# Optimization experiments

Measured on AMD Instinct MI355X. Metric: run time of the kernel, lower is better.

Reference implementation:

```python
import jax, jax.numpy as jnp
import numpy as np

N, E, DIN, DH, DC = 50000, 1600000, 128, 128, 40
EPS = 1e-5  # BatchNorm eps


def _seg_sum(v, idx, n):
    return jax.ops.segment_sum(v, idx, num_segments=n)


def setup_inputs() -> dict:
    key = jax.random.key(0)
    ks = jax.random.split(key, 24)
    rn = lambda i, shp, s=0.05: jax.random.normal(ks[i], shp, jnp.float32) * s
    return {
        "x": jax.random.normal(ks[0], (N, DIN), jnp.float32),
        "src": jax.random.randint(ks[1], (E,), 0, N, jnp.int32),
        "dst": jax.random.randint(ks[2], (E,), 0, N, jnp.int32),
        # CoNet layer 1 (in -> hidden)
        "w11s": rn(3, (DIN, DH)), "w11n": rn(4, (DIN, DH)), "b11": jnp.zeros((DH,), jnp.float32),
        "w12": rn(5, (DIN, DH)), "b12": jnp.zeros((DH,), jnp.float32),
        "w13": rn(6, (DIN, DH)), "a13l": rn(7, (DH,)), "a13r": rn(8, (DH,)), "b13": jnp.zeros((DH,), jnp.float32),
        "cw1": jax.random.uniform(ks[9], (3,), jnp.float32, 0.5, 1.5),
        # BatchNorm1d
        "g": jnp.ones((DH,), jnp.float32), "be": jnp.zeros((DH,), jnp.float32),
        # CoNet layer 2 (hidden -> out)
        "w21s": rn(10, (DH, DC)), "w21n": rn(11, (DH, DC)), "b21": jnp.zeros((DC,), jnp.float32),
        "w22": rn(12, (DH, DC)), "b22": jnp.zeros((DC,), jnp.float32),
        "w23": rn(13, (DH, DC)), "a23l": rn(14, (DC,)), "a23r": rn(15, (DC,)), "b23": jnp.zeros((DC,), jnp.float32),
        "cw2": jax.random.uniform(ks[16], (3,), jnp.float32, 0.5, 1.5),
    }


def conet(x, src, dst, ws, wn, bs, wg, bg, wa, al, ar, ba, cw):
    """AFFN CoNet: SAGE(mean) + GCN + GAT(1 head), fused by normalized weights."""
    n = x.shape[0]
    ones = jnp.ones((src.shape[0],), x.dtype)
    indeg = _seg_sum(ones, dst, n)   # in-degree per node
    outdeg = _seg_sum(ones, src, n)  # out-degree per node

    # --- SAGEConv, mean aggregator: fc_self(x) + fc_neigh(mean_neigh(x)) ---
    nei = _seg_sum(x[src], dst, n) / jnp.maximum(indeg, 1.0)[:, None]
    x1 = x @ ws + nei @ wn + bs

    ns = jnp.maximum(outdeg, 1.0) ** -0.5
    nd = jnp.maximum(indeg, 1.0) ** -0.5
    h = _seg_sum((x * ns[:, None])[src], dst, n) * nd[:, None]
    x2 = h @ wg + bg

    # --- GATConv, 1 head ---
    f = x @ wa                       # [N, out]
    el = f @ al                      # [N]
    er = f @ ar                      # [N]
    e = jax.nn.leaky_relu(el[src] + er[dst], 0.2)  # [E]
    m = jax.ops.segment_max(e, dst, num_segments=n)
    a = jnp.exp(e - m[dst])
    s = _seg_sum(a, dst, n)
    alpha = a / jnp.maximum(s[dst], 1e-9)
    x3 = _seg_sum(alpha[:, None] * f[src], dst, n) + ba

    w = cw / jnp.sum(cw)
    return w[0] * x1 + w[1] * x2 + w[2] * x3


def reference(x, src, dst,
              w11s, w11n, b11, w12, b12, w13, a13l, a13r, b13, cw1,
              g, be,
              w21s, w21n, b21, w22, b22, w23, a23l, a23r, b23, cw2):
    h = conet(x, src, dst, w11s, w11n, b11, w12, b12, w13, a13l, a13r, b13, cw1)
    # BatchNorm1d (training-mode batch statistics)
    mu = jnp.mean(h, axis=0)
    var = jnp.var(h, axis=0)
    h = (h - mu) * jax.lax.rsqrt(var + EPS) * g + be
    h = jax.nn.relu(h)
    # dropout in eval mode: identity
    h = conet(h, src, dst, w21s, w21n, b21, w22, b22, w23, a23l, a23r, b23, cw2)
    return jax.nn.log_softmax(h, axis=1)
```

## Files before the change

### kernel.cpp

```cpp
#include <hip/hip_runtime.h>
#include <hip/hip_bf16.h>
#include <math.h>

#define DIN 128
#define DH  128
#define DC  40

#define HCHUNK  12544
#define NSTRIPE 128
#define NPAD    (HCHUNK * 4)

typedef unsigned short u16;
typedef unsigned int u32;
typedef unsigned char u8;
typedef __attribute__((ext_vector_type(2))) float f32x2;
typedef __attribute__((ext_vector_type(4))) float f32x4;
typedef __attribute__((ext_vector_type(8))) short bf16x8;

static __device__ __forceinline__ float bf2f(u16 u) {
    union { u32 i; float f; } v; v.i = ((u32)u) << 16; return v.f;
}
static __device__ __forceinline__ u16 f2bf(float f) {
    __hip_bfloat16 h = __float2bfloat16(f);
    union { __hip_bfloat16 h; u16 u; } v; v.h = h; return v.u;
}
static __device__ __forceinline__ u32 pack2bf(float a, float b) {
    return ((u32)f2bf(b) << 16) | (u32)f2bf(a);
}

static __device__ __forceinline__ u8 f2fp8(float f) {
    u32 s = (__float_as_uint(f) >> 31) << 7;
    float a = fabsf(f);
    a = fminf(a, 448.f);
    if (a < 0.015625f) {
        int q = (int)rintf(a * 512.f);
        return (u8)(s | (u32)q);
    }
    u32 x = __float_as_uint(a);
    u32 lsb = (x >> 20) & 1;
    x += 0x0007FFFF + lsb;
    u32 e = (x >> 23) - 120;
    u32 m = (x >> 20) & 7;
    return (u8)(s | (e << 3) | m);
}

#if __has_builtin(__builtin_amdgcn_cvt_pk_f32_fp8)
template<bool HI>
static __device__ __forceinline__ f32x2 fp8pk(u32 w) {
    return __builtin_amdgcn_cvt_pk_f32_fp8((int)w, HI);
}
#else
static __device__ __forceinline__ float fp8dec1(u32 byte) {
    u32 s = (byte >> 7) & 1, em = byte & 0x7F;
    float v = __uint_as_float((s << 31) | (em << 20)) * 0x1p120f;
    return v;
}
template<bool HI>
static __device__ __forceinline__ f32x2 fp8pk(u32 w) {
    u32 b0 = HI ? ((w >> 16) & 0xff) : (w & 0xff);
    u32 b1 = HI ? ((w >> 24) & 0xff) : ((w >> 8) & 0xff);
    f32x2 r; r.x = fp8dec1(b0); r.y = fp8dec1(b1); return r;
}
#endif

__global__ __launch_bounds__(256) void k_hist(const int* __restrict__ key,
        u16* __restrict__ partials, u16* __restrict__ wsrank, int E, int eps, int writeRank) {
    __shared__ u32 hist[HCHUNK];
    int chunk = blockIdx.x;
    int stripe = blockIdx.y;
    int base = chunk * (HCHUNK * 2);
    for (int i = threadIdx.x; i < HCHUNK; i += 256) hist[i] = 0;
    __syncthreads();
    int e0 = stripe * eps;
    int e1 = e0 + eps; if (e1 > E) e1 = E;
    for (int e = e0 + threadIdx.x; e < e1; e += 256) {
        int k = key[e] - base;
        if ((u32)k < (u32)(HCHUNK * 2)) {
            u32 old = atomicAdd(&hist[k >> 1], 1u << ((k & 1) * 16));
            if (writeRank) wsrank[e] = (u16)((old >> ((k & 1) * 16)) & 0xffff);
        }
    }
    __syncthreads();
    u32* prow = (u32*)(partials + (size_t)stripe * NPAD + base);
    for (int i = threadIdx.x; i < HCHUNK; i += 256) prow[i] = hist[i];
}

__global__ void k_pfx(u16* __restrict__ partials, int* __restrict__ deg,
                      float* __restrict__ nsOut, int n) {
    int node = blockIdx.x * 256 + threadIdx.x;
    if (node >= NPAD) return;
    int run = 0;
    for (int s0 = 0; s0 < NSTRIPE; s0 += 16) {
        u16 c[16];
#pragma unroll
        for (int i = 0; i < 16; ++i) c[i] = partials[(size_t)(s0 + i) * NPAD + node];
#pragma unroll
        for (int i = 0; i < 16; ++i) {
            partials[(size_t)(s0 + i) * NPAD + node] = (u16)run;
            run += c[i];
        }
    }
    if (node < n) {
        deg[node] = run;
        if (nsOut) {
            int d = run < 1 ? 1 : run;
            nsOut[node] = rsqrtf((float)d);
        }
    }
}

__global__ void k_scan1(const int* __restrict__ deg, int* __restrict__ excl,
                        int* __restrict__ bsum, int n) {
    __shared__ int sh[256];
    int i = blockIdx.x * 256 + threadIdx.x;
    int v = (i < n) ? deg[i] : 0;
    sh[threadIdx.x] = v; __syncthreads();
    for (int o = 1; o < 256; o <<= 1) {
        int t = (threadIdx.x >= o) ? sh[threadIdx.x - o] : 0;
        __syncthreads(); sh[threadIdx.x] += t; __syncthreads();
    }
    if (i < n) excl[i] = sh[threadIdx.x] - v;
    if (threadIdx.x == 255) bsum[blockIdx.x] = sh[255];
}
__global__ void k_scan2(int* __restrict__ bsum, int nb) {
    __shared__ int sh[256];
    int t = threadIdx.x;
    int v = (t < nb) ? bsum[t] : 0;
    sh[t] = v; __syncthreads();
    for (int o = 1; o < 256; o <<= 1) {
        int u = (t >= o) ? sh[t - o] : 0;
        __syncthreads(); sh[t] += u; __syncthreads();
    }
    if (t < nb) bsum[t] = sh[t] - v;
}
__global__ void k_scan3(const int* __restrict__ excl, const int* __restrict__ bsum,
                        int* __restrict__ rowptr, int n, int E) {
    int i = blockIdx.x * 256 + threadIdx.x;
    if (i < n) rowptr[i] = excl[i] + bsum[blockIdx.x];
    if (i == 0) rowptr[n] = E;
}

__global__ __launch_bounds__(256) void k_place2(const int* __restrict__ src,
        const int* __restrict__ dst, const int* __restrict__ rowptr,
        const u16* __restrict__ partials, const u16* __restrict__ wsrank,
        int* __restrict__ col, int E, int eps) {
    int stripe = blockIdx.x;
    const u16* prow = partials + (size_t)stripe * NPAD;
    int sub = (eps + 3) >> 2;
    int e0 = stripe * eps + blockIdx.y * sub;
    int e1 = e0 + sub;
    int cap = stripe * eps + eps; if (cap > E) cap = E;
    if (e1 > cap) e1 = cap;
    for (int e = e0 + threadIdx.x; e < e1; e += 256) {
        int d = dst[e];
        col[rowptr[d] + prow[d] + wsrank[e]] = src[e];
    }
}

__global__ void k_w1(const float* w11s, const float* w11n, const float* w12, const float* w13,
                     const float* b11, const float* b12, const float* b13, const float* cw,
                     u16* __restrict__ Wf, float* __restrict__ bc) {
    int i = blockIdx.x * blockDim.x + threadIdx.x;
    float s = cw[0] + cw[1] + cw[2];
    float w0 = cw[0] / s, w1 = cw[1] / s, w2 = cw[2] / s;
    if (i < 16 * 8 * 64 * 8) {
        int j = i & 7, lane = (i >> 3) & 63, nt = (i >> 9) & 7, kt = i >> 12;
        int k = kt * 32 + ((lane >> 4) << 3) + j;
        int n = nt * 16 + (lane & 15);
        float v;
        if (k < 128)      v = w0 * w11s[k * 128 + n];
        else if (k < 256) v = w0 * w11n[(k - 128) * 128 + n];
        else if (k < 384) v = w1 * w12[(k - 256) * 128 + n];
        else              v = w2 * w13[(k - 384) * 128 + n];
        Wf[i] = f2bf(v);
    }
    if (i < 128) bc[i] = w0 * b11[i] + w1 * b12[i] + w2 * b13[i];
}

__global__ void k_w2(const float* w21s, const float* w21n, const float* w22, const float* w23,
                     const float* b21, const float* b22, const float* b23, const float* cw,
                     u16* __restrict__ Wf, float* __restrict__ bc) {
    int i = blockIdx.x * blockDim.x + threadIdx.x;
    float s = cw[0] + cw[1] + cw[2];
    float w0 = cw[0] / s, w1 = cw[1] / s, w2 = cw[2] / s;
    if (i < 16 * 3 * 64 * 8) {
        int j = i & 7;
        int l2 = i >> 3;
        int lane = l2 & 63;
        int t2 = l2 >> 6;
        int nt = t2 % 3, kt = t2 / 3;
        int k = kt * 32 + ((lane >> 4) << 3) + j;
        int n = nt * 16 + (lane & 15);
        float v = 0.f;
        if (n < 40) {
            if (k < 128)      v = w0 * w21s[k * 40 + n];
            else if (k < 256) v = w0 * w21n[(k - 128) * 40 + n];
            else if (k < 384) v = w1 * w22[(k - 256) * 40 + n];
            else              v = w2 * w23[(k - 384) * 40 + n];
        }
        Wf[i] = f2bf(v);
    }
    if (i < 40) bc[i] = w0 * b21[i] + w1 * b22[i] + w2 * b23[i];
}

__global__ void k_attn(const float* w13, const float* a13l, const float* a13r,
                       const float* w23, const float* a23l, const float* a23r,
                       float* __restrict__ v) {
    int t = blockIdx.x * blockDim.x + threadIdx.x;
    if (t < 128) {
        float s = 0; for (int j = 0; j < 128; ++j) s += w13[t * 128 + j] * a13l[j];
        v[t] = s;
    } else if (t < 256) {
        int i = t - 128; float s = 0; for (int j = 0; j < 128; ++j) s += w13[i * 128 + j] * a13r[j];
        v[t] = s;
    } else if (t < 384) {
        int i = t - 256; float s = 0; for (int j = 0; j < 40; ++j) s += w23[i * 40 + j] * a23l[j];
        v[t] = s;
    } else if (t < 512) {
        int i = t - 384; float s = 0; for (int j = 0; j < 40; ++j) s += w23[i * 40 + j] * a23r[j];
        v[t] = s;
    }
}

__global__ __launch_bounds__(256) void k_cvt_dots(const float* __restrict__ X,
        const float* __restrict__ vl, const float* __restrict__ vr, const float* __restrict__ ns,
        u16* __restrict__ Xb, u8* __restrict__ Xq,
        float2* __restrict__ elns, float* __restrict__ er, int n) {
    int w = (blockIdx.x * blockDim.x + threadIdx.x) >> 6;
    int lane = threadIdx.x & 63;
    if (w >= n) return;
    float2 xv = *(const float2*)&X[(size_t)w * 128 + lane * 2];
    *(u32*)&Xb[(size_t)w * 128 + lane * 2] = pack2bf(xv.x, xv.y);
    u16 q = (u16)f2fp8(xv.x) | ((u16)f2fp8(xv.y) << 8);
    *(u16*)&Xq[(size_t)w * 128 + lane * 2] = q;
    float2 a = *(const float2*)&vl[lane * 2];
    float2 b = *(const float2*)&vr[lane * 2];
    float dl = xv.x * a.x + xv.y * a.y;
    float dr = xv.x * b.x + xv.y * b.y;
    for (int off = 32; off; off >>= 1) {
        dl += __shfl_down(dl, off);
        dr += __shfl_down(dr, off);
    }
    if (lane == 0) { elns[w] = make_float2(dl, ns[w]); er[w] = dr; }
}

__global__ __launch_bounds__(256) void k_agg(const u8* __restrict__ Xq,
        const int* __restrict__ rowptr, const int* __restrict__ colsrc,
        const float2* __restrict__ elns, const float* __restrict__ er,
        u16* __restrict__ AG, int n) {
    int w = (blockIdx.x * blockDim.x + threadIdx.x) >> 6;
    int lane = threadIdx.x & 63;
    if (w >= n) return;
    int g = lane >> 4, gl = lane & 15;
    int beg = rowptr[w], end = rowptr[w + 1];
    int k = end - beg;
    float erd = er[w];
    f32x2 aS2[4] = {}, aG2[4] = {}, aA2[4] = {};
    float m = -INFINITY, ssum = 0.f;
    for (int c0 = beg; c0 < end; c0 += 64) {
        int cnt = end - c0; if (cnt > 64) cnt = 64;
        int s = 0; float e = -INFINITY; float nsl = 0.f;
        if (lane < cnt) {
            s = colsrc[c0 + lane];
            float2 v = elns[s];
            float t = v.x + erd;
            e = t > 0.f ? t : 0.2f * t;
            nsl = v.y;
        }
        float cm = e;
        for (int o = 32; o; o >>= 1) cm = fmaxf(cm, __shfl_xor(cm, o));
        float nm = fmaxf(m, cm);
        float scale = __expf(m - nm);
        float p = (lane < cnt) ? __expf(e - nm) : 0.f;
        float ps = p;
        for (int o = 32; o; o >>= 1) ps += __shfl_xor(ps, o);
        ssum = ssum * scale + ps;
        f32x2 scale2 = {scale, scale};
#pragma unroll
        for (int i = 0; i < 4; ++i) aA2[i] *= scale2;
        m = nm;
        int full = cnt >> 2;
#pragma unroll 8
        for (int t = 0; t < full; ++t) {
            int j = (t << 2) + g;
            int sj = __shfl(s, j);
            float pj = __shfl(p, j);
            float nsj = __shfl(nsl, j);
            uint2 xq = *(const uint2*)&Xq[(size_t)sj * 128 + gl * 8];
            f32x2 xv2[4] = {fp8pk<false>(xq.x), fp8pk<true>(xq.x),
                            fp8pk<false>(xq.y), fp8pk<true>(xq.y)};
            f32x2 ns2 = {nsj, nsj}, p2 = {pj, pj};
#pragma unroll
            for (int q = 0; q < 4; ++q) {
                aS2[q] += xv2[q];
                aG2[q] += ns2 * xv2[q];
                aA2[q] += p2 * xv2[q];
            }
        }
        if (cnt & 3) {
            int j = (full << 2) + g;
            int sj = __shfl(s, j);
            float pj = __shfl(p, j);
            float nsj = __shfl(nsl, j);
            if (j < cnt) {
                uint2 xq = *(const uint2*)&Xq[(size_t)sj * 128 + gl * 8];
                f32x2 xv2[4] = {fp8pk<false>(xq.x), fp8pk<true>(xq.x),
                                fp8pk<false>(xq.y), fp8pk<true>(xq.y)};
                f32x2 ns2 = {nsj, nsj}, p2 = {pj, pj};
#pragma unroll
                for (int q = 0; q < 4; ++q) {
                    aS2[q] += xv2[q];
                    aG2[q] += ns2 * xv2[q];
                    aA2[q] += p2 * xv2[q];
                }
            }
        }
    }
    float aS[8], aG[8], aA[8];
#pragma unroll
    for (int i = 0; i < 4; ++i) {
        aS[2 * i] = aS2[i][0]; aS[2 * i + 1] = aS2[i][1];
        aG[2 * i] = aG2[i][0]; aG[2 * i + 1] = aG2[i][1];
        aA[2 * i] = aA2[i][0]; aA[2 * i + 1] = aA2[i][1];
    }
#pragma unroll
    for (int i = 0; i < 8; ++i) {
        aS[i] += __shfl_xor(aS[i], 16); aS[i] += __shfl_xor(aS[i], 32);
        aG[i] += __shfl_xor(aG[i], 16); aG[i] += __shfl_xor(aG[i], 32);
        aA[i] += __shfl_xor(aA[i], 16); aA[i] += __shfl_xor(aA[i], 32);
    }
    int kc = k < 1 ? 1 : k;
    float invk = 1.f / (float)kc;
    float ndd = rsqrtf((float)kc);
    float gi = 1.f / fmaxf(ssum, 1e-9f);
    u16* row = AG + (size_t)w * 384;
    if (g == 0) {
        uint4 o = make_uint4(pack2bf(aS[0] * invk, aS[1] * invk), pack2bf(aS[2] * invk, aS[3] * invk),
                             pack2bf(aS[4] * invk, aS[5] * invk), pack2bf(aS[6] * invk, aS[7] * invk));
        *(uint4*)&row[gl * 8] = o;
    } else if (g == 1) {
        uint4 o = make_uint4(pack2bf(aG[0] * ndd, aG[1] * ndd), pack2bf(aG[2] * ndd, aG[3] * ndd),
                             pack2bf(aG[4] * ndd, aG[5] * ndd), pack2bf(aG[6] * ndd, aG[7] * ndd));
        *(uint4*)&row[128 + gl * 8] = o;
    } else if (g == 2) {
        uint4 o = make_uint4(pack2bf(aA[0] * gi, aA[1] * gi), pack2bf(aA[2] * gi, aA[3] * gi),
                             pack2bf(aA[4] * gi, aA[5] * gi), pack2bf(aA[6] * gi, aA[7] * gi));
        *(uint4*)&row[256 + gl * 8] = o;
    }
}

__global__ __launch_bounds__(256) void k_gemm1(const u16* __restrict__ Xb,
        const u16* __restrict__ AG, const u16* __restrict__ Wf,
        const float* __restrict__ bias, u16* __restrict__ C, int M) {
    const int NT = 8;
    int wave = threadIdx.x >> 6;
    int lane = threadIdx.x & 63;
    int m0 = blockIdx.x * 64 + wave * 16;
    int arow = m0 + (lane & 15);
    if (arow >= M) arow = M - 1;
    int kq = lane >> 4;
    f32x4 acc[NT];
#pragma unroll
    for (int t = 0; t < NT; ++t) acc[t] = (f32x4){0.f, 0.f, 0.f, 0.f};
#pragma unroll
    for (int kt = 0; kt < 16; ++kt) {
        int k0 = kt * 32 + kq * 8;
        bf16x8 a;
        if (k0 < 128) a = *(const bf16x8*)&Xb[(size_t)arow * 128 + k0];
        else          a = *(const bf16x8*)&AG[(size_t)arow * 384 + (k0 - 128)];
        const u16* wb = Wf + ((size_t)kt * NT) * 512 + lane * 8;
#pragma unroll
        for (int t = 0; t < NT; ++t) {
            bf16x8 b = *(const bf16x8*)&wb[(size_t)t * 512];
            acc[t] = __builtin_amdgcn_mfma_f32_16x16x32_bf16(a, b, acc[t], 0, 0, 0);
        }
    }
    int ccol = lane & 15;
    int rbase = m0 + kq * 4;
#pragma unroll
    for (int t = 0; t < NT; ++t) {
        int col = t * 16 + ccol;
        float bv = bias[col];
#pragma unroll
        for (int r = 0; r < 4; ++r) {
            int rr = rbase + r;
            if (rr < M) C[(size_t)rr * 128 + col] = f2bf(acc[t][r] + bv);
        }
    }
}

__global__ __launch_bounds__(256) void k_gemm2_lsm(const u16* __restrict__ Xb,
        const u16* __restrict__ AG, const u16* __restrict__ Wf,
        const float* __restrict__ bias, float* __restrict__ out, int M) {
    const int NT = 3;
    int wave = threadIdx.x >> 6;
    int lane = threadIdx.x & 63;
    int m0 = blockIdx.x * 64 + wave * 16;
    int arow = m0 + (lane & 15);
    if (arow >= M) arow = M - 1;
    int kq = lane >> 4;
    f32x4 acc[NT];
#pragma unroll
    for (int t = 0; t < NT; ++t) acc[t] = (f32x4){0.f, 0.f, 0.f, 0.f};
#pragma unroll
    for (int kt = 0; kt < 16; ++kt) {
        int k0 = kt * 32 + kq * 8;
        bf16x8 a;
        if (k0 < 128) a = *(const bf16x8*)&Xb[(size_t)arow * 128 + k0];
        else          a = *(const bf16x8*)&AG[(size_t)arow * 384 + (k0 - 128)];
        const u16* wb = Wf + ((size_t)kt * NT) * 512 + lane * 8;
#pragma unroll
        for (int t = 0; t < NT; ++t) {
            bf16x8 b = *(const bf16x8*)&wb[(size_t)t * 512];
            acc[t] = __builtin_amdgcn_mfma_f32_16x16x32_bf16(a, b, acc[t], 0, 0, 0);
        }
    }
    int ccol = lane & 15;
    int rbase = m0 + kq * 4;
    bool valid[NT];
    float bv[NT];
#pragma unroll
    for (int t = 0; t < NT; ++t) {
        int col = t * 16 + ccol;
        valid[t] = (col < 40);
        bv[t] = valid[t] ? bias[col] : 0.f;
    }
#pragma unroll
    for (int r = 0; r < 4; ++r) {
        float v[NT];
#pragma unroll
        for (int t = 0; t < NT; ++t) v[t] = valid[t] ? (acc[t][r] + bv[t]) : -INFINITY;
        float mx = fmaxf(fmaxf(v[0], v[1]), v[2]);
        for (int o = 1; o < 16; o <<= 1) mx = fmaxf(mx, __shfl_xor(mx, o));
        float se = 0.f;
#pragma unroll
        for (int t = 0; t < NT; ++t) se += valid[t] ? __expf(v[t] - mx) : 0.f;
        for (int o = 1; o < 16; o <<= 1) se += __shfl_xor(se, o);
        float lse = mx + logf(se);
        int rr = rbase + r;
        if (rr < M) {
#pragma unroll
            for (int t = 0; t < NT; ++t) {
                int col = t * 16 + ccol;
                if (valid[t]) out[(size_t)rr * 40 + col] = v[t] - lse;
            }
        }
    }
}

__global__ __launch_bounds__(256) void k_bn_stats(const u16* __restrict__ H,
        float* __restrict__ acc, int nrows) {
    int c = threadIdx.x & 127;
    int rh = threadIdx.x >> 7;
    int r0 = blockIdx.x * 256;
    int rend = r0 + 256; if (rend > nrows) rend = nrows;
    float s = 0.f, q = 0.f;
    for (int r = r0 + rh; r < rend; r += 2) {
        float v = bf2f(H[(size_t)r * 128 + c]);
        s += v; q += v * v;
    }
    atomicAdd(&acc[c], s);
    atomicAdd(&acc[128 + c], q);
}

__global__ void k_bn_final(const float* __restrict__ acc, const float* __restrict__ g,
                           const float* __restrict__ be, float* __restrict__ scsh, float n) {
    int c = threadIdx.x;
    float mu = acc[c] / n;
    float var = acc[128 + c] / n - mu * mu;
    float sc = g[c] * rsqrtf(var + 1e-5f);
    scsh[c] = sc;
    scsh[128 + c] = be[c] - mu * sc;
}

__global__ __launch_bounds__(256) void k_bnorm_dots(const u16* __restrict__ Hp,
        const float* __restrict__ scsh, const float* __restrict__ vl, const float* __restrict__ vr,
        const float* __restrict__ ns,
        u16* __restrict__ H, u8* __restrict__ H8,
        float2* __restrict__ elns, float* __restrict__ er, int n) {
    int w = (blockIdx.x * blockDim.x + threadIdx.x) >> 6;
    int lane = threadIdx.x & 63;
    if (w >= n) return;
    u32 hu = *(const u32*)&Hp[(size_t)w * 128 + lane * 2];
    float vx = bf2f((u16)hu), vy = bf2f((u16)(hu >> 16));
    float2 sc = *(const float2*)&scsh[lane * 2];
    float2 sh = *(const float2*)&scsh[128 + lane * 2];
    float h0 = fmaxf(vx * sc.x + sh.x, 0.f);
    float h1 = fmaxf(vy * sc.y + sh.y, 0.f);
    *(u32*)&H[(size_t)w * 128 + lane * 2] = pack2bf(h0, h1);
    u16 q = (u16)f2fp8(h0) | ((u16)f2fp8(h1) << 8);
    *(u16*)&H8[(size_t)w * 128 + lane * 2] = q;
    float2 a = *(const float2*)&vl[lane * 2];
    float2 b = *(const float2*)&vr[lane * 2];
    float dl = h0 * a.x + h1 * a.y;
    float dr = h0 * b.x + h1 * b.y;
    for (int off = 32; off; off >>= 1) {
        dl += __shfl_down(dl, off);
        dr += __shfl_down(dr, off);
    }
    if (lane == 0) { elns[w] = make_float2(dl, ns[w]); er[w] = dr; }
}

extern "C" void kernel_launch(void* const* d_in, const int* in_sizes, int n_in,
                              void* d_out, int out_size, void* d_ws, size_t ws_size,
                              hipStream_t stream) {
    const float* x    = (const float*)d_in[0];
    const int*   src  = (const int*)d_in[1];
    const int*   dst  = (const int*)d_in[2];
    const float* w11s = (const float*)d_in[3];
    const float* w11n = (const float*)d_in[4];
    const float* b11  = (const float*)d_in[5];
    const float* w12  = (const float*)d_in[6];
    const float* b12  = (const float*)d_in[7];
    const float* w13  = (const float*)d_in[8];
    const float* a13l = (const float*)d_in[9];
    const float* a13r = (const float*)d_in[10];
    const float* b13  = (const float*)d_in[11];
    const float* cw1  = (const float*)d_in[12];
    const float* g    = (const float*)d_in[13];
    const float* be   = (const float*)d_in[14];
    const float* w21s = (const float*)d_in[15];
    const float* w21n = (const float*)d_in[16];
    const float* b21  = (const float*)d_in[17];
    const float* w22  = (const float*)d_in[18];
    const float* b22  = (const float*)d_in[19];
    const float* w23  = (const float*)d_in[20];
    const float* a23l = (const float*)d_in[21];
    const float* a23r = (const float*)d_in[22];
    const float* b23  = (const float*)d_in[23];
    const float* cw2  = (const float*)d_in[24];

    const int N = in_sizes[0] / DIN;
    const int E = in_sizes[1];

    char* ws = (char*)d_ws;
    size_t off = 0;
    auto alloc = [&](size_t bytes) { size_t o = off; off += (bytes + 255) & ~(size_t)255; return o; };
    u16*   Xb     = (u16*)(ws + alloc((size_t)N * 128 * 2));
    u8*    Xq     = (u8*)(ws + alloc((size_t)N * 128));
    u16*   AG     = (u16*)(ws + alloc((size_t)N * 384 * 2));
    u16*   hpre   = (u16*)(ws + alloc((size_t)N * 128 * 2));
    u16*   h      = (u16*)(ws + alloc((size_t)N * 128 * 2));
    u8*    h8     = (u8*)(ws + alloc((size_t)N * 128));
    int*   col    = (int*)(ws + alloc((size_t)E * 4));
    u16*   wsrank = (u16*)(ws + alloc((size_t)E * 2));
    u16*   partials = (u16*)(ws + alloc((size_t)NSTRIPE * NPAD * 2));
    int*   rowptr = (int*)(ws + alloc((size_t)(N + 1) * 4));
    int*   indeg  = (int*)(ws + alloc((size_t)N * 4));
    int*   outdeg = (int*)(ws + alloc((size_t)N * 4));
    int*   excl   = (int*)(ws + alloc((size_t)N * 4));
    int*   bsum   = (int*)(ws + alloc(256 * 4));
    float* ns     = (float*)(ws + alloc((size_t)N * 4));
    float2* elns  = (float2*)(ws + alloc((size_t)N * 8));
    float* er     = (float*)(ws + alloc((size_t)N * 4));
    u16*   Wf1    = (u16*)(ws + alloc((size_t)16 * 8 * 64 * 8 * 2));
    u16*   Wf2    = (u16*)(ws + alloc((size_t)16 * 3 * 64 * 8 * 2));
    float* bc1    = (float*)(ws + alloc(128 * 4));
    float* bc2    = (float*)(ws + alloc(40 * 4));
    float* vattn  = (float*)(ws + alloc(512 * 4));
    float* bnacc  = (float*)(ws + alloc(256 * 4));
    float* scsh   = (float*)(ws + alloc(256 * 4));

    (void)hipMemsetAsync(bnacc, 0, 256 * 4, stream);

    int eb_eps = (E + NSTRIPE - 1) / NSTRIPE;
    int wb = (N * 64 + 255) / 256;
    int sb = (N + 255) / 256;
    int gb = (N + 63) / 64;
    int pb = (NPAD + 255) / 256;

    k_w1<<<(16 * 8 * 64 * 8 + 255) / 256, 256, 0, stream>>>(w11s, w11n, w12, w13, b11, b12, b13, cw1, Wf1, bc1);
    k_w2<<<(16 * 3 * 64 * 8 + 255) / 256, 256, 0, stream>>>(w21s, w21n, w22, w23, b21, b22, b23, cw2, Wf2, bc2);
    k_attn<<<2, 256, 0, stream>>>(w13, a13l, a13r, w23, a23l, a23r, vattn);

    {
        dim3 hg(2, NSTRIPE);
        k_hist<<<hg, 256, 0, stream>>>(src, partials, wsrank, E, eb_eps, 0);
        k_pfx<<<pb, 256, 0, stream>>>(partials, outdeg, ns, N);
        k_hist<<<hg, 256, 0, stream>>>(dst, partials, wsrank, E, eb_eps, 1);
        k_pfx<<<pb, 256, 0, stream>>>(partials, indeg, (float*)nullptr, N);
        k_scan1<<<sb, 256, 0, stream>>>(indeg, excl, bsum, N);
        k_scan2<<<1, 256, 0, stream>>>(bsum, sb);
        k_scan3<<<sb, 256, 0, stream>>>(excl, bsum, rowptr, N, E);
        dim3 pg(NSTRIPE, 4);
        k_place2<<<pg, 256, 0, stream>>>(src, dst, rowptr, partials, wsrank, col, E, eb_eps);
    }

    k_cvt_dots<<<wb, 256, 0, stream>>>(x, vattn, vattn + 128, ns, Xb, Xq, elns, er, N);
    k_agg<<<wb, 256, 0, stream>>>(Xq, rowptr, col, elns, er, AG, N);
    k_gemm1<<<gb, 256, 0, stream>>>(Xb, AG, Wf1, bc1, hpre, N);

    k_bn_stats<<<(N + 255) / 256, 256, 0, stream>>>(hpre, bnacc, N);
    k_bn_final<<<1, 128, 0, stream>>>(bnacc, g, be, scsh, (float)N);
    k_bnorm_dots<<<wb, 256, 0, stream>>>(hpre, scsh, vattn + 256, vattn + 384, ns, h, h8, elns, er, N);

    k_agg<<<wb, 256, 0, stream>>>(h8, rowptr, col, elns, er, AG, N);
    k_gemm2_lsm<<<gb, 256, 0, stream>>>(h, AG, Wf2, bc2, (float*)d_out, N);
}
```

Baseline: 457.2 us.

## Fuse prep, histogram and prefix kernels; drop online softmax max; fold BN finalize

Merges the weight/bias/attention-vector prep kernels into one launch, computes src and dst histograms in a single pass with two LDS tables, and merges the two prefix passes. The GAT aggregation now exponentiates leaky-relu logits directly without a running max and rescaling, removing shuffle reductions per chunk. BatchNorm finalize is recomputed inside the normalize kernel, and the accumulator zeroing moves into the GEMM kernel, removing a memset and a launch. Risks: larger LDS per hist block lowers occupancy, and skipping the max subtraction can overflow exp for large logits.

```diff
diff --git a/kernel.cpp b/kernel.cpp
--- a/kernel.cpp
+++ b/kernel.cpp
@@ -63,49 +63,126 @@
 }
 #endif
 
-__global__ __launch_bounds__(256) void k_hist(const int* __restrict__ key,
-        u16* __restrict__ partials, u16* __restrict__ wsrank, int E, int eps, int writeRank) {
-    __shared__ u32 hist[HCHUNK];
+__global__ __launch_bounds__(256) void k_prep(
+        const float* w11s, const float* w11n, const float* w12, const float* w13,
+        const float* b11, const float* b12, const float* b13, const float* cw1,
+        const float* w21s, const float* w21n, const float* w22, const float* w23,
+        const float* b21, const float* b22, const float* b23, const float* cw2,
+        const float* a13l, const float* a13r, const float* a23l, const float* a23r,
+        u16* __restrict__ Wf1, u16* __restrict__ Wf2,
+        float* __restrict__ bc1, float* __restrict__ bc2, float* __restrict__ vattn) {
+    int i = blockIdx.x * 256 + threadIdx.x;
+    float s1 = cw1[0] + cw1[1] + cw1[2];
+    float u0 = cw1[0] / s1, u1 = cw1[1] / s1, u2 = cw1[2] / s1;
+    float s2 = cw2[0] + cw2[1] + cw2[2];
+    float q0 = cw2[0] / s2, q1 = cw2[1] / s2, q2 = cw2[2] / s2;
+    if (i < 65536) {
+        int j = i & 7, lane = (i >> 3) & 63, nt = (i >> 9) & 7, kt = i >> 12;
+        int k = kt * 32 + ((lane >> 4) << 3) + j;
+        int n = nt * 16 + (lane & 15);
+        float v;
+        if (k < 128)      v = u0 * w11s[k * 128 + n];
+        else if (k < 256) v = u0 * w11n[(k - 128) * 128 + n];
+        else if (k < 384) v = u1 * w12[(k - 256) * 128 + n];
+        else              v = u2 * w13[(k - 384) * 128 + n];
+        Wf1[i] = f2bf(v);
+    } else if (i < 90112) {
+        int i2 = i - 65536;
+        int j = i2 & 7;
+        int l2 = i2 >> 3;
+        int lane = l2 & 63;
+        int t2 = l2 >> 6;
+        int nt = t2 % 3, kt = t2 / 3;
+        int k = kt * 32 + ((lane >> 4) << 3) + j;
+        int n = nt * 16 + (lane & 15);
+        float v = 0.f;
+        if (n < 40) {
+            if (k < 128)      v = q0 * w21s[k * 40 + n];
+            else if (k < 256) v = q0 * w21n[(k - 128) * 40 + n];
+            else if (k < 384) v = q1 * w22[(k - 256) * 40 + n];
+            else              v = q2 * w23[(k - 384) * 40 + n];
+        }
+        Wf2[i2] = f2bf(v);
+    } else if (i < 90624) {
+        int t = i - 90112;
+        if (t < 128) {
+            float s = 0; for (int j = 0; j < 128; ++j) s += w13[t * 128 + j] * a13l[j];
+            vattn[t] = s;
+        } else if (t < 256) {
+            int r = t - 128; float s = 0; for (int j = 0; j < 128; ++j) s += w13[r * 128 + j] * a13r[j];
+            vattn[t] = s;
+        } else if (t < 384) {
+            int r = t - 256; float s = 0; for (int j = 0; j < 40; ++j) s += w23[r * 40 + j] * a23l[j];
+            vattn[t] = s;
+        } else {
+            int r = t - 384; float s = 0; for (int j = 0; j < 40; ++j) s += w23[r * 40 + j] * a23r[j];
+            vattn[t] = s;
+        }
+    } else if (i < 90752) {
+        int c = i - 90624;
+        bc1[c] = u0 * b11[c] + u1 * b12[c] + u2 * b13[c];
+    } else if (i < 90792) {
+        int c = i - 90752;
+        bc2[c] = q0 * b21[c] + q1 * b22[c] + q2 * b23[c];
+    }
+}
+
+__global__ __launch_bounds__(256) void k_hist2(const int* __restrict__ src,
+        const int* __restrict__ dst,
+        u16* __restrict__ partialsS, u16* __restrict__ partialsD,
+        u16* __restrict__ wsrank, int E, int eps) {
+    __shared__ u32 histS[HCHUNK];
+    __shared__ u32 histD[HCHUNK];
     int chunk = blockIdx.x;
     int stripe = blockIdx.y;
     int base = chunk * (HCHUNK * 2);
-    for (int i = threadIdx.x; i < HCHUNK; i += 256) hist[i] = 0;
+    for (int i = threadIdx.x; i < HCHUNK; i += 256) { histS[i] = 0; histD[i] = 0; }
     __syncthreads();
     int e0 = stripe * eps;
     int e1 = e0 + eps; if (e1 > E) e1 = E;
     for (int e = e0 + threadIdx.x; e < e1; e += 256) {
-        int k = key[e] - base;
-        if ((u32)k < (u32)(HCHUNK * 2)) {
-            u32 old = atomicAdd(&hist[k >> 1], 1u << ((k & 1) * 16));
-            if (writeRank) wsrank[e] = (u16)((old >> ((k & 1) * 16)) & 0xffff);
+        int ks = src[e] - base;
+        int kd = dst[e] - base;
+        if ((u32)ks < (u32)(HCHUNK * 2))
+            atomicAdd(&histS[ks >> 1], 1u << ((ks & 1) * 16));
+        if ((u32)kd < (u32)(HCHUNK * 2)) {
+            u32 old = atomicAdd(&histD[kd >> 1], 1u << ((kd & 1) * 16));
+            wsrank[e] = (u16)((old >> ((kd & 1) * 16)) & 0xffff);
         }
     }
     __syncthreads();
-    u32* prow = (u32*)(partials + (size_t)stripe * NPAD + base);
-    for (int i = threadIdx.x; i < HCHUNK; i += 256) prow[i] = hist[i];
-}
-
-__global__ void k_pfx(u16* __restrict__ partials, int* __restrict__ deg,
-                      float* __restrict__ nsOut, int n) {
+    u32* prowS = (u32*)(partialsS + (size_t)stripe * NPAD + base);
+    u32* prowD = (u32*)(partialsD + (size_t)stripe * NPAD + base);
+    for (int i = threadIdx.x; i < HCHUNK; i += 256) { prowS[i] = histS[i]; prowD[i] = histD[i]; }
+}
+
+__global__ void k_pfx2(const u16* __restrict__ partialsS, u16* __restrict__ partialsD,
+                       int* __restrict__ indeg, float* __restrict__ ns, int n) {
     int node = blockIdx.x * 256 + threadIdx.x;
     if (node >= NPAD) return;
-    int run = 0;
+    int runS = 0;
     for (int s0 = 0; s0 < NSTRIPE; s0 += 16) {
         u16 c[16];
 #pragma unroll
-        for (int i = 0; i < 16; ++i) c[i] = partials[(size_t)(s0 + i) * NPAD + node];
+        for (int i = 0; i < 16; ++i) c[i] = partialsS[(size_t)(s0 + i) * NPAD + node];
+#pragma unroll
+        for (int i = 0; i < 16; ++i) runS += c[i];
+    }
+    int runD = 0;
+    for (int s0 = 0; s0 < NSTRIPE; s0 += 16) {
+        u16 c[16];
+#pragma unroll
+        for (int i = 0; i < 16; ++i) c[i] = partialsD[(size_t)(s0 + i) * NPAD + node];
 #pragma unroll
         for (int i = 0; i < 16; ++i) {
-            partials[(size_t)(s0 + i) * NPAD + node] = (u16)run;
-            run += c[i];
+            partialsD[(size_t)(s0 + i) * NPAD + node] = (u16)runD;
+            runD += c[i];
         }
     }
     if (node < n) {
-        deg[node] = run;
-        if (nsOut) {
-            int d = run < 1 ? 1 : run;
-            nsOut[node] = rsqrtf((float)d);
-        }
+        indeg[node] = runD;
+        int d = runS < 1 ? 1 : runS;
+        ns[node] = rsqrtf((float)d);
     }
 }
 
@@ -154,71 +231,6 @@
     for (int e = e0 + threadIdx.x; e < e1; e += 256) {
         int d = dst[e];
         col[rowptr[d] + prow[d] + wsrank[e]] = src[e];
-    }
-}
-
-__global__ void k_w1(const float* w11s, const float* w11n, const float* w12, const float* w13,
-                     const float* b11, const float* b12, const float* b13, const float* cw,
-                     u16* __restrict__ Wf, float* __restrict__ bc) {
-    int i = blockIdx.x * blockDim.x + threadIdx.x;
-    float s = cw[0] + cw[1] + cw[2];
-    float w0 = cw[0] / s, w1 = cw[1] / s, w2 = cw[2] / s;
-    if (i < 16 * 8 * 64 * 8) {
-        int j = i & 7, lane = (i >> 3) & 63, nt = (i >> 9) & 7, kt = i >> 12;
-        int k = kt * 32 + ((lane >> 4) << 3) + j;
-        int n = nt * 16 + (lane & 15);
-        float v;
-        if (k < 128)      v = w0 * w11s[k * 128 + n];
-        else if (k < 256) v = w0 * w11n[(k - 128) * 128 + n];
-        else if (k < 384) v = w1 * w12[(k - 256) * 128 + n];
-        else              v = w2 * w13[(k - 384) * 128 + n];
-        Wf[i] = f2bf(v);
-    }
-    if (i < 128) bc[i] = w0 * b11[i] + w1 * b12[i] + w2 * b13[i];
-}
-
-__global__ void k_w2(const float* w21s, const float* w21n, const float* w22, const float* w23,
-                     const float* b21, const float* b22, const float* b23, const float* cw,
-                     u16* __restrict__ Wf, float* __restrict__ bc) {
-    int i = blockIdx.x * blockDim.x + threadIdx.x;
-    float s = cw[0] + cw[1] + cw[2];
-    float w0 = cw[0] / s, w1 = cw[1] / s, w2 = cw[2] / s;
-    if (i < 16 * 3 * 64 * 8) {
-        int j = i & 7;
-        int l2 = i >> 3;
-        int lane = l2 & 63;
-        int t2 = l2 >> 6;
-        int nt = t2 % 3, kt = t2 / 3;
-        int k = kt * 32 + ((lane >> 4) << 3) + j;
-        int n = nt * 16 + (lane & 15);
-        float v = 0.f;
-        if (n < 40) {
-            if (k < 128)      v = w0 * w21s[k * 40 + n];
-            else if (k < 256) v = w0 * w21n[(k - 128) * 40 + n];
-            else if (k < 384) v = w1 * w22[(k - 256) * 40 + n];
-            else              v = w2 * w23[(k - 384) * 40 + n];
-        }
-        Wf[i] = f2bf(v);
-    }
-    if (i < 40) bc[i] = w0 * b21[i] + w1 * b22[i] + w2 * b23[i];
-}
-
-__global__ void k_attn(const float* w13, const float* a13l, const float* a13r,
-                       const float* w23, const float* a23l, const float* a23r,
-                       float* __restrict__ v) {
-    int t = blockIdx.x * blockDim.x + threadIdx.x;
-    if (t < 128) {
-        float s = 0; for (int j = 0; j < 128; ++j) s += w13[t * 128 + j] * a13l[j];
-        v[t] = s;
-    } else if (t < 256) {
-        int i = t - 128; float s = 0; for (int j = 0; j < 128; ++j) s += w13[i * 128 + j] * a13r[j];
-        v[t] = s;
-    } else if (t < 384) {
-        int i = t - 256; float s = 0; for (int j = 0; j < 40; ++j) s += w23[i * 40 + j] * a23l[j];
-        v[t] = s;
-    } else if (t < 512) {
-        int i = t - 384; float s = 0; for (int j = 0; j < 40; ++j) s += w23[i * 40 + j] * a23r[j];
-        v[t] = s;
     }
 }
 
@@ -256,29 +268,21 @@
     int k = end - beg;
     float erd = er[w];
     f32x2 aS2[4] = {}, aG2[4] = {}, aA2[4] = {};
-    float m = -INFINITY, ssum = 0.f;
+    float ssum = 0.f;
     for (int c0 = beg; c0 < end; c0 += 64) {
         int cnt = end - c0; if (cnt > 64) cnt = 64;
-        int s = 0; float e = -INFINITY; float nsl = 0.f;
+        int s = 0; float p = 0.f; float nsl = 0.f;
         if (lane < cnt) {
             s = colsrc[c0 + lane];
             float2 v = elns[s];
             float t = v.x + erd;
-            e = t > 0.f ? t : 0.2f * t;
+            t = t > 0.f ? t : 0.2f * t;
+            p = __expf(t);
             nsl = v.y;
         }
-        float cm = e;
-        for (int o = 32; o; o >>= 1) cm = fmaxf(cm, __shfl_xor(cm, o));
-        float nm = fmaxf(m, cm);
-        float scale = __expf(m - nm);
-        float p = (lane < cnt) ? __expf(e - nm) : 0.f;
         float ps = p;
         for (int o = 32; o; o >>= 1) ps += __shfl_xor(ps, o);
-        ssum = ssum * scale + ps;
-        f32x2 scale2 = {scale, scale};
-#pragma unroll
-        for (int i = 0; i < 4; ++i) aA2[i] *= scale2;
-        m = nm;
+        ssum += ps;
         int full = cnt >> 2;
 #pragma unroll 8
         for (int t = 0; t < full; ++t) {
@@ -351,7 +355,9 @@
 
 __global__ __launch_bounds__(256) void k_gemm1(const u16* __restrict__ Xb,
         const u16* __restrict__ AG, const u16* __restrict__ Wf,
-        const float* __restrict__ bias, u16* __restrict__ C, int M) {
+        const float* __restrict__ bias, u16* __restrict__ C,
+        float* __restrict__ bnacc, int M) {
+    if (blockIdx.x == 0 && threadIdx.x < 256) bnacc[threadIdx.x] = 0.f;
     const int NT = 8;
     int wave = threadIdx.x >> 6;
     int lane = threadIdx.x & 63;
@@ -463,30 +469,27 @@
     atomicAdd(&acc[128 + c], q);
 }
 
-__global__ void k_bn_final(const float* __restrict__ acc, const float* __restrict__ g,
-                           const float* __restrict__ be, float* __restrict__ scsh, float n) {
-    int c = threadIdx.x;
-    float mu = acc[c] / n;
-    float var = acc[128 + c] / n - mu * mu;
-    float sc = g[c] * rsqrtf(var + 1e-5f);
-    scsh[c] = sc;
-    scsh[128 + c] = be[c] - mu * sc;
-}
-
 __global__ __launch_bounds__(256) void k_bnorm_dots(const u16* __restrict__ Hp,
-        const float* __restrict__ scsh, const float* __restrict__ vl, const float* __restrict__ vr,
+        const float* __restrict__ bnacc, const float* __restrict__ g, const float* __restrict__ be,
+        const float* __restrict__ vl, const float* __restrict__ vr,
         const float* __restrict__ ns,
         u16* __restrict__ H, u8* __restrict__ H8,
-        float2* __restrict__ elns, float* __restrict__ er, int n) {
+        float2* __restrict__ elns, float* __restrict__ er, float Nf, int n) {
     int w = (blockIdx.x * blockDim.x + threadIdx.x) >> 6;
     int lane = threadIdx.x & 63;
     if (w >= n) return;
+    int c0 = lane * 2, c1 = lane * 2 + 1;
+    float mu0 = bnacc[c0] / Nf, mu1 = bnacc[c1] / Nf;
+    float var0 = bnacc[128 + c0] / Nf - mu0 * mu0;
+    float var1 = bnacc[128 + c1] / Nf - mu1 * mu1;
+    float sc0 = g[c0] * rsqrtf(var0 + 1e-5f);
+    float sc1 = g[c1] * rsqrtf(var1 + 1e-5f);
+    float sh0 = be[c0] - mu0 * sc0;
+    float sh1 = be[c1] - mu1 * sc1;
     u32 hu = *(const u32*)&Hp[(size_t)w * 128 + lane * 2];
     float vx = bf2f((u16)hu), vy = bf2f((u16)(hu >> 16));
-    float2 sc = *(const float2*)&scsh[lane * 2];
-    float2 sh = *(const float2*)&scsh[128 + lane * 2];
-    float h0 = fmaxf(vx * sc.x + sh.x, 0.f);
-    float h1 = fmaxf(vy * sc.y + sh.y, 0.f);
+    float h0 = fmaxf(vx * sc0 + sh0, 0.f);
+    float h1 = fmaxf(vy * sc1 + sh1, 0.f);
     *(u32*)&H[(size_t)w * 128 + lane * 2] = pack2bf(h0, h1);
     u16 q = (u16)f2fp8(h0) | ((u16)f2fp8(h1) << 8);
     *(u16*)&H8[(size_t)w * 128 + lane * 2] = q;
@@ -544,10 +547,10 @@
     u8*    h8     = (u8*)(ws + alloc((size_t)N * 128));
     int*   col    = (int*)(ws + alloc((size_t)E * 4));
     u16*   wsrank = (u16*)(ws + alloc((size_t)E * 2));
-    u16*   partials = (u16*)(ws + alloc((size_t)NSTRIPE * NPAD * 2));
+    u16*   partialsS = (u16*)(ws + alloc((size_t)NSTRIPE * NPAD * 2));
+    u16*   partialsD = (u16*)(ws + alloc((size_t)NSTRIPE * NPAD * 2));
     int*   rowptr = (int*)(ws + alloc((size_t)(N + 1) * 4));
     int*   indeg  = (int*)(ws + alloc((size_t)N * 4));
-    int*   outdeg = (int*)(ws + alloc((size_t)N * 4));
     int*   excl   = (int*)(ws + alloc((size_t)N * 4));
     int*   bsum   = (int*)(ws + alloc(256 * 4));
     float* ns     = (float*)(ws + alloc((size_t)N * 4));
@@ -559,9 +562,6 @@
     float* bc2    = (float*)(ws + alloc(40 * 4));
     float* vattn  = (float*)(ws + alloc(512 * 4));
     float* bnacc  = (float*)(ws + alloc(256 * 4));
-    float* scsh   = (float*)(ws + alloc(256 * 4));
-
-    (void)hipMemsetAsync(bnacc, 0, 256 * 4, stream);
 
     int eb_eps = (E + NSTRIPE - 1) / NSTRIPE;
     int wb = (N * 64 + 255) / 256;
@@ -569,30 +569,29 @@
     int gb = (N + 63) / 64;
     int pb = (NPAD + 255) / 256;
 
-    k_w1<<<(16 * 8 * 64 * 8 + 255) / 256, 256, 0, stream>>>(w11s, w11n, w12, w13, b11, b12, b13, cw1, Wf1, bc1);
-    k_w2<<<(16 * 3 * 64 * 8 + 255) / 256, 256, 0, stream>>>(w21s, w21n, w22, w23, b21, b22, b23, cw2, Wf2, bc2);
-    k_attn<<<2, 256, 0, stream>>>(w13, a13l, a13r, w23, a23l, a23r, vattn);
+    k_prep<<<(90792 + 255) / 256, 256, 0, stream>>>(
+        w11s, w11n, w12, w13, b11, b12, b13, cw1,
+        w21s, w21n, w22, w23, b21, b22, b23, cw2,
+        a13l, a13r, a23l, a23r, Wf1, Wf2, bc1, bc2, vattn);
 
     {
         dim3 hg(2, NSTRIPE);
-        k_hist<<<hg, 256, 0, stream>>>(src, partials, wsrank, E, eb_eps, 0);
-        k_pfx<<<pb, 256, 0, stream>>>(partials, outdeg, ns, N);
-        k_hist<<<hg, 256, 0, stream>>>(dst, partials, wsrank, E, eb_eps, 1);
-        k_pfx<<<pb, 256, 0, stream>>>(partials, indeg, (float*)nullptr, N);
+        k_hist2<<<hg, 256, 0, stream>>>(src, dst, partialsS, partialsD, wsrank, E, eb_eps);
+        k_pfx2<<<pb, 256, 0, stream>>>(partialsS, partialsD, indeg, ns, N);
         k_scan1<<<sb, 256, 0, stream>>>(indeg, excl, bsum, N);
         k_scan2<<<1, 256, 0, stream>>>(bsum, sb);
         k_scan3<<<sb, 256, 0, stream>>>(excl, bsum, rowptr, N, E);
         dim3 pg(NSTRIPE, 4);
-        k_place2<<<pg, 256, 0, stream>>>(src, dst, rowptr, partials, wsrank, col, E, eb_eps);
+        k_place2<<<pg, 256, 0, stream>>>(src, dst, rowptr, partialsD, wsrank, col, E, eb_eps);
     }
 
     k_cvt_dots<<<wb, 256, 0, stream>>>(x, vattn, vattn + 128, ns, Xb, Xq, elns, er, N);
     k_agg<<<wb, 256, 0, stream>>>(Xq, rowptr, col, elns, er, AG, N);
-    k_gemm1<<<gb, 256, 0, stream>>>(Xb, AG, Wf1, bc1, hpre, N);
+    k_gemm1<<<gb, 256, 0, stream>>>(Xb, AG, Wf1, bc1, hpre, bnacc, N);
 
     k_bn_stats<<<(N + 255) / 256, 256, 0, stream>>>(hpre, bnacc, N);
-    k_bn_final<<<1, 128, 0, stream>>>(bnacc, g, be, scsh, (float)N);
-    k_bnorm_dots<<<wb, 256, 0, stream>>>(hpre, scsh, vattn + 256, vattn + 384, ns, h, h8, elns, er, N);
+    k_bnorm_dots<<<wb, 256, 0, stream>>>(hpre, bnacc, g, be, vattn + 256, vattn + 384, ns,
+                                         h, h8, elns, er, (float)N, N);
 
     k_agg<<<wb, 256, 0, stream>>>(h8, rowptr, col, elns, er, AG, N);
     k_gemm2_lsm<<<gb, 256, 0, stream>>>(h, AG, Wf2, bc2, (float*)d_out, N);
```

After: 426.3 us. 6.8% less time.
